# Optimization experiments

Hardware: AMD Instinct MI355X
Metric: run time of the kernel (lower is better)

The kernel has to match this reference:

```python
import jax, jax.numpy as jnp
import numpy as np

PROPOSAL_COUNT = 100
IOU_THRESHOLD = 0.5
SCORE_THRESHOLD = 0.05
IGNORE_LABEL = 0
PERFORMANCE_COUNT = 4096

B, N, C = 4, 100000, 80


def setup_inputs() -> dict:
    key = jax.random.key(0)
    k1, k2, k3, k4 = jax.random.split(key, 4)
    logits = jax.random.uniform(k1, (B, N, C), dtype=jnp.float32)
    regress = jax.random.uniform(k2, (B, N, 4), dtype=jnp.float32)
    points = jax.random.uniform(k3, (N, 2), dtype=jnp.float32)
    centerness = jax.random.uniform(k4, (B, N, 1), dtype=jnp.float32)
    return {"logits": logits, "regress": regress, "points": points, "centerness": centerness}


def offset2bbox(points, regress):
    return jnp.concatenate([points - regress[..., :2], points + regress[..., 2:]], axis=-1)


def pairwise_iou(boxes):
    # boxes: [K, 4] -> iou [K, K]
    area = (boxes[:, 2] - boxes[:, 0]) * (boxes[:, 3] - boxes[:, 1])
    lt = jnp.maximum(boxes[:, None, :2], boxes[None, :, :2])
    rb = jnp.minimum(boxes[:, None, 2:], boxes[None, :, 2:])
    wh = jnp.clip(rb - lt, 0.0)
    inter = wh[..., 0] * wh[..., 1]
    union = area[:, None] + area[None, :] - inter
    return inter / jnp.maximum(union, 1e-9)


def nms_image(logit, box):
    # logit: [N, C] (centerness-fused scores), box: [N, 4] decoded+clipped boxes
    n, c = logit.shape
    score = logit.at[:, IGNORE_LABEL].set(0.0)            # drop background class
    score = jnp.where(score > SCORE_THRESHOLD, score, 0.0)
    top_s, top_i = jax.lax.top_k(score.reshape(-1), PERFORMANCE_COUNT)  # over N*C pairs
    anchor = top_i // c
    cls = top_i % c
    cboxes = box[anchor]                                   # [K, 4]
    iou = pairwise_iou(cboxes)                             # [K, K]
    suppress = (iou > IOU_THRESHOLD) & (cls[:, None] == cls[None, :])

    def body(i, state):
        valid, sel = state
        s = jnp.where(valid, top_s, -1.0)
        j = jnp.argmax(s)
        ok = s[j] > 0.0
        sel = sel.at[i].set(jnp.where(ok, j.astype(jnp.int32), -1))
        valid = valid & ~suppress[j]
        valid = valid.at[j].set(False)
        return valid, sel

    valid0 = top_s > 0.0
    sel0 = jnp.full((PROPOSAL_COUNT,), -1, jnp.int32)
    _, sel = jax.lax.fori_loop(0, PROPOSAL_COUNT, body, (valid0, sel0))
    ok = sel >= 0
    selc = jnp.maximum(sel, 0)
    out_logit = jnp.where(ok[:, None], logit[anchor[selc]], 0.0)  # [P, C]
    out_box = jnp.where(ok[:, None], cboxes[selc], 0.0)           # [P, 4]
    return out_logit, out_box


def reference(logits, regress, points, centerness):
    fused = jnp.sqrt(logits * centerness)                        # centerness fusion
    boxes = jnp.clip(offset2bbox(points[None, :, :], regress), 0.0, 1.0)
    out_logit, out_box = jax.vmap(nms_image)(fused, boxes)
    return out_logit, out_box
```

## Files before the change

### kernel.cpp

```cpp
#include <hip/hip_runtime.h>
#include <cstdint>
#include <cstddef>

#define BB 4
#define NN 100000
#define CC 80
#define NC (NN * CC)
#define KTOP 4096
#define PROP 100
#define HBINS 10248
#define BUCKET_BASE 0x3D000u
#define CAPB 16384
#define SPILLCAP 131072
#define T0BK 0x3F733u
#define SPILL_LO (T0BK - BUCKET_BASE)
#define SPILL_BINS (HBINS - SPILL_LO)
#define P1CAP 1024
#define NSEL 512

#define HIST_BYTES (BB * HBINS * 4)
#define CTRL_OFF   HIST_BYTES
#define ZERO_BYTES (HIST_BYTES + 128)
#define CANDA_OFF  (HIST_BYTES + 128)
#define CANDB_OFF  (CANDA_OFF + BB * KTOP * 8)
#define SPILL_OFF  (CANDB_OFF + BB * CAPB * 8)
#define WS_NEEDED  ((size_t)SPILL_OFF + (size_t)BB * SPILLCAP * 8)

__device__ __forceinline__ void agg_push(bool pred, unsigned long long pk,
                                         unsigned* counter, unsigned long long* buf,
                                         unsigned cap, int lane) {
    unsigned long long m = __ballot(pred);
    if (m) {
        int leader = __ffsll(m) - 1;
        unsigned base = 0;
        if (lane == leader) base = atomicAdd(counter, (unsigned)__popcll(m));
        base = (unsigned)__shfl((int)base, leader);
        if (pred) {
            unsigned pos = base + (unsigned)__popcll(m & ((1ull << lane) - 1ull));
            if (pos < cap) buf[pos] = pk;
        }
    }
}

__global__ void k_pass1(const float* __restrict__ logits, const float* __restrict__ cent,
                        unsigned* __restrict__ ctrl, unsigned long long* __restrict__ spill) {
    int b = blockIdx.y;
    __shared__ unsigned long long lbuf[P1CAP];
    __shared__ unsigned lcnt, gbase, lflush;
    if (threadIdx.x == 0) lcnt = 0;
    __syncthreads();
    const float4* lg = (const float4*)(logits + (size_t)b * NC);
    const float* cb = cent + (size_t)b * NN;
    const int T4 = NC / 4;
    for (int i = blockIdx.x * blockDim.x + threadIdx.x; i < T4; i += gridDim.x * blockDim.x) {
        float4 v = lg[i];
        int n = i / 20;
        int c4 = (i - n * 20) * 4;
        float ce = cb[n];
        unsigned k0 = __float_as_uint(sqrtf(v.x * ce));
        unsigned k1 = __float_as_uint(sqrtf(v.y * ce));
        unsigned k2 = __float_as_uint(sqrtf(v.z * ce));
        unsigned k3 = __float_as_uint(sqrtf(v.w * ce));
        bool p0 = (c4 != 0) && ((k0 >> 12) >= T0BK);
        bool p1 = (k1 >> 12) >= T0BK;
        bool p2 = (k2 >> 12) >= T0BK;
        bool p3 = (k3 >> 12) >= T0BK;
        unsigned cnt = (unsigned)p0 + (unsigned)p1 + (unsigned)p2 + (unsigned)p3;
        if (cnt) {
            unsigned q = atomicAdd(&lcnt, cnt);
            unsigned f = (unsigned)i * 4u;
            if (p0) { if (q < P1CAP) lbuf[q] = ((unsigned long long)k0 << 32) | (unsigned)(~(f + 0)); q++; }
            if (p1) { if (q < P1CAP) lbuf[q] = ((unsigned long long)k1 << 32) | (unsigned)(~(f + 1)); q++; }
            if (p2) { if (q < P1CAP) lbuf[q] = ((unsigned long long)k2 << 32) | (unsigned)(~(f + 2)); q++; }
            if (p3) { if (q < P1CAP) lbuf[q] = ((unsigned long long)k3 << 32) | (unsigned)(~(f + 3)); }
        }
    }
    __syncthreads();
    if (threadIdx.x == 0) {
        unsigned n = lcnt;
        if (n > P1CAP) { atomicOr(&ctrl[6], 1u); n = P1CAP; }
        lflush = n;
        gbase = n ? atomicAdd(&ctrl[b * 8 + 4], n) : 0u;
    }
    __syncthreads();
    unsigned long long* sp = spill + (size_t)b * SPILLCAP;
    unsigned n = lflush, g0 = gbase;
    for (unsigned i = threadIdx.x; i < n; i += blockDim.x) {
        unsigned pos = g0 + i;
        if (pos < SPILLCAP) sp[pos] = lbuf[i];
    }
}

__global__ void k_slowflag(unsigned* __restrict__ ctrl) {
    if (threadIdx.x == 0 && blockIdx.x == 0) {
        unsigned f = ctrl[6] ? 1u : 0u;
        for (int b = 0; b < BB; b++) {
            unsigned ns = ctrl[b * 8 + 4];
            if (ns < KTOP || ns > SPILLCAP) f = 1;
        }
        ctrl[7] = f;
    }
}

__global__ void k_hist_spill(const unsigned* __restrict__ ctrl,
                             const unsigned long long* __restrict__ spill,
                             unsigned* __restrict__ hist) {
    if (ctrl[7]) return;
    int b = blockIdx.y;
    __shared__ unsigned lh[SPILL_BINS];
    for (int i = threadIdx.x; i < SPILL_BINS; i += blockDim.x) lh[i] = 0;
    __syncthreads();
    unsigned ns = ctrl[b * 8 + 4];
    if (ns > SPILLCAP) ns = SPILLCAP;
    const unsigned long long* sp = spill + (size_t)b * SPILLCAP;
    for (unsigned i = blockIdx.x * blockDim.x + threadIdx.x; i < ns; i += gridDim.x * blockDim.x) {
        unsigned bits = (unsigned)(sp[i] >> 32);
        atomicAdd(&lh[(bits >> 12) - T0BK], 1u);
    }
    __syncthreads();
    unsigned* gh = hist + (size_t)b * HBINS + SPILL_LO;
    for (int i = threadIdx.x; i < SPILL_BINS; i += blockDim.x) {
        unsigned c = lh[i];
        if (c) atomicAdd(&gh[i], c);
    }
}

__global__ void k_hist(const float* __restrict__ logits, const float* __restrict__ cent,
                       unsigned* __restrict__ hist, const unsigned* __restrict__ ctrl) {
    if (ctrl[7] == 0) return;
    int b = blockIdx.y;
    __shared__ unsigned lh[HBINS];
    for (int i = threadIdx.x; i < HBINS; i += blockDim.x) lh[i] = 0;
    __syncthreads();
    const float4* lg = (const float4*)(logits + (size_t)b * NC);
    const float* cb = cent + (size_t)b * NN;
    const int T4 = NC / 4;
    for (int i = blockIdx.x * blockDim.x + threadIdx.x; i < T4; i += gridDim.x * blockDim.x) {
        float4 v = lg[i];
        int n = i / 20;
        int c4 = (i - n * 20) * 4;
        float ce = cb[n];
        float s;
        s = sqrtf(v.x * ce);
        if (c4 != 0 && s > 0.05f) atomicAdd(&lh[(__float_as_uint(s) >> 12) - BUCKET_BASE], 1u);
        s = sqrtf(v.y * ce);
        if (s > 0.05f) atomicAdd(&lh[(__float_as_uint(s) >> 12) - BUCKET_BASE], 1u);
        s = sqrtf(v.z * ce);
        if (s > 0.05f) atomicAdd(&lh[(__float_as_uint(s) >> 12) - BUCKET_BASE], 1u);
        s = sqrtf(v.w * ce);
        if (s > 0.05f) atomicAdd(&lh[(__float_as_uint(s) >> 12) - BUCKET_BASE], 1u);
    }
    __syncthreads();
    unsigned* gh = hist + (size_t)b * HBINS;
    for (int i = threadIdx.x; i < HBINS; i += blockDim.x) {
        unsigned c = lh[i];
        if (c) atomicAdd(&gh[i], c);
    }
}

__global__ void k_select(const unsigned* __restrict__ hist, unsigned* __restrict__ ctrl) {
    int b = blockIdx.x;
    int t = threadIdx.x;
    const unsigned* h = hist + (size_t)b * HBINS;
    __shared__ unsigned ssum[256];
    const int CH = (HBINS + 255) / 256;
    unsigned acc0 = 0;
    for (int i = 0; i < CH; i++) {
        int idx = t * CH + i;
        if (idx < HBINS) acc0 += h[idx];
    }
    ssum[t] = acc0;
    __syncthreads();
    for (int off = 1; off < 256; off <<= 1) {
        unsigned v = (t + off < 256) ? ssum[t + off] : 0u;
        __syncthreads();
        ssum[t] += v;
        __syncthreads();
    }
    unsigned acc = (t < 255) ? ssum[t + 1] : 0u;
    for (int i = CH - 1; i >= 0; i--) {
        int idx = t * CH + i;
        if (idx >= HBINS) continue;
        unsigned cnt = h[idx];
        unsigned na = acc + cnt;
        if (na >= KTOP && acc < KTOP) {
            ctrl[b * 8 + 0] = (unsigned)idx;
            ctrl[b * 8 + 1] = acc;
        }
        acc = na;
    }
}

__global__ void k_compact_fast(unsigned* __restrict__ ctrl,
                               const unsigned long long* __restrict__ spill,
                               unsigned long long* __restrict__ candA,
                               unsigned long long* __restrict__ candB) {
    if (ctrl[7]) return;
    int b = blockIdx.y;
    unsigned B1 = ctrl[b * 8 + 0];
    unsigned ns = ctrl[b * 8 + 4];
    if (ns > SPILLCAP) ns = SPILLCAP;
    const unsigned long long* sp = spill + (size_t)b * SPILLCAP;
    unsigned long long* gA = candA + (size_t)b * KTOP;
    unsigned long long* gB = candB + (size_t)b * CAPB;
    int lane = threadIdx.x & 63;
    unsigned TT = gridDim.x * blockDim.x;
    unsigned iters = (ns + TT - 1) / TT;
    for (unsigned k2 = 0; k2 < iters; k2++) {
        unsigned i = k2 * TT + blockIdx.x * blockDim.x + threadIdx.x;
        bool active = (i < ns);
        unsigned long long pk = active ? sp[i] : 0ull;
        unsigned bk = active ? (((unsigned)(pk >> 32)) >> 12) - BUCKET_BASE : 0u;
        bool pA = active && (bk > B1);
        bool pB = active && (bk == B1);
        agg_push(pA, pk, &ctrl[b * 8 + 2], gA, KTOP, lane);
        agg_push(pB, pk, &ctrl[b * 8 + 3], gB, CAPB, lane);
    }
}

__global__ void k_compact(const float* __restrict__ logits, const float* __restrict__ cent,
                          unsigned* __restrict__ ctrl,
                          unsigned long long* __restrict__ candA,
                          unsigned long long* __restrict__ candB) {
    if (ctrl[7] == 0) return;
    int b = blockIdx.y;
    unsigned B1 = ctrl[b * 8 + 0];
    const float4* lg = (const float4*)(logits + (size_t)b * NC);
    const float* cb = cent + (size_t)b * NN;
    const int T4 = NC / 4;
    unsigned long long* gA = candA + (size_t)b * KTOP;
    unsigned long long* gB = candB + (size_t)b * CAPB;
    for (int i = blockIdx.x * blockDim.x + threadIdx.x; i < T4; i += gridDim.x * blockDim.x) {
        float4 v = lg[i];
        int n = i / 20;
        int c4 = (i - n * 20) * 4;
        float ce = cb[n];
        float sv[4] = {v.x, v.y, v.z, v.w};
#pragma unroll
        for (int k = 0; k < 4; k++) {
            float s = sqrtf(sv[k] * ce);
            int c = c4 + k;
            if (c != 0 && s > 0.05f) {
                unsigned key = __float_as_uint(s);
                unsigned bk = (key >> 12) - BUCKET_BASE;
                if (bk >= B1) {
                    unsigned flat = (unsigned)(i * 4 + k);
                    unsigned long long pk = ((unsigned long long)key << 32) | (unsigned)(~flat);
                    if (bk > B1) {
                        unsigned p = atomicAdd(&ctrl[b * 8 + 2], 1u);
                        if (p < KTOP) gA[p] = pk;
                    } else {
                        unsigned p = atomicAdd(&ctrl[b * 8 + 3], 1u);
                        if (p < CAPB) gB[p] = pk;
                    }
                }
            }
        }
    }
}

__global__ void k_boundary(unsigned* __restrict__ ctrl,
                           unsigned long long* __restrict__ candA,
                           const unsigned long long* __restrict__ candB) {
    int b = blockIdx.x;
    int t = threadIdx.x;
    unsigned nA = ctrl[b * 8 + 2];
    if (nA > KTOP) nA = KTOP;
    unsigned nB = ctrl[b * 8 + 3];
    if (nB > CAPB) nB = CAPB;
    int m = (int)KTOP - (int)nA;
    if (m < 0) m = 0;
    __shared__ unsigned long long sB[8192];
    const unsigned long long* gB = candB + (size_t)b * CAPB;
    unsigned long long* gA = candA + (size_t)b * KTOP;
    unsigned nBr = (nB + 255u) & ~255u;
    for (unsigned ii = 0; ii < nBr; ii += 256) {
        unsigned i = ii + (unsigned)t;
        bool act = (i < nB);
        unsigned long long ki = act ? gB[i] : 0ull;
        unsigned rank = 0;
        for (unsigned cb0 = 0; cb0 < nB; cb0 += 8192) {
            unsigned chunk = nB - cb0;
            if (chunk > 8192) chunk = 8192;
            __syncthreads();
            for (unsigned j = (unsigned)t; j < chunk; j += 256) sB[j] = gB[cb0 + j];
            __syncthreads();
            if (act) {
                for (unsigned j = 0; j < chunk; j++) rank += (sB[j] > ki) ? 1u : 0u;
            }
        }
        if (act && rank < (unsigned)m) gA[nA + rank] = ki;
    }
    unsigned take = ((unsigned)m < nB) ? (unsigned)m : nB;
    unsigned filled = nA + take;
    for (unsigned i = filled + (unsigned)t; i < KTOP; i += 256) gA[i] = 0ull;
}

__global__ void __launch_bounds__(256, 1) k_nms(const float* __restrict__ logits,
                                                const float* __restrict__ regress,
                                                const float* __restrict__ points,
                                                const float* __restrict__ cent,
                                                const unsigned long long* __restrict__ candA,
                                                float* __restrict__ out) {
    int b = blockIdx.x;
    int t = threadIdx.x;
    const unsigned long long* gA = candA + (size_t)b * KTOP;

    __shared__ unsigned long long sk[KTOP];
    __shared__ unsigned long long sel[KTOP];
    __shared__ float4 sbox[KTOP];
    __shared__ unsigned hist2[SPILL_BINS];
    __shared__ unsigned sc[8];
    __shared__ float4 kbox[PROP];
    __shared__ unsigned selAnc[PROP];

    for (int i = t; i < SPILL_BINS; i += 256) hist2[i] = 0;
    if (t < 8) sc[t] = 0;
    __syncthreads();
    for (int i = t; i < KTOP; i += 256) {
        unsigned long long kk = gA[i];
        sk[i] = kk;
        if (kk) {
            int bkt = (int)((unsigned)(kk >> 32) >> 12) - (int)T0BK;
            bkt = bkt < 0 ? 0 : bkt;
            atomicAdd(&hist2[bkt], 1u);
            atomicAdd(&sc[0], 1u);
        }
    }
    __syncthreads();

    for (int round = 0; round < 2; round++) {
        unsigned target = round == 0 ? NSEL : KTOP;
        if (t == 0) {
            unsigned total = sc[0];
            unsigned tgt = target < total ? target : total;
            int bq = SPILL_BINS;
            if (tgt > 0) {
                unsigned acc = 0;
                for (int i = SPILL_BINS - 1; i >= 0; i--) {
                    acc += hist2[i];
                    if (acc >= tgt) { bq = i; break; }
                }
            }
            sc[2] = (unsigned)bq;
            sc[1] = 0;
            sc[3] = 0;
            sc[4] = 0;
        }
        __syncthreads();
        int bq = (int)sc[2];
        for (int i = t; i < KTOP; i += 256) {
            unsigned long long kk = sk[i];
            if (kk) {
                int bkt = (int)((unsigned)(kk >> 32) >> 12) - (int)T0BK;
                bkt = bkt < 0 ? 0 : bkt;
                if (bkt >= bq) {
                    unsigned p = atomicAdd(&sc[1], 1u);
                    sel[p] = kk;
                }
            }
        }
        __syncthreads();
        unsigned S = sc[1];
        unsigned P2 = 2;
        while (P2 < S) P2 <<= 1;
        for (unsigned i = S + t; i < P2; i += 256) sel[i] = 0ull;
        __syncthreads();
        for (unsigned k = 2; k <= P2; k <<= 1) {
            for (unsigned j = k >> 1; j > 0; j >>= 1) {
                for (unsigned t2 = t; t2 < P2 / 2; t2 += 256) {
                    unsigned i = ((t2 & ~(j - 1)) << 1) | (t2 & (j - 1));
                    unsigned p2i = i + j;
                    bool dir = ((i & k) == 0);
                    unsigned long long a = sel[i], c = sel[p2i];
                    if ((a < c) == dir) { sel[i] = c; sel[p2i] = a; }
                }
                __syncthreads();
            }
        }
        for (unsigned i = t; i < S; i += 256) {
            unsigned long long kk = sel[i];
            float4 bx = {0.f, 0.f, 0.f, 0.f};
            if (kk) {
                unsigned flat = ~(unsigned)kk;
                unsigned a = flat / CC;
                float px = points[a * 2 + 0], py = points[a * 2 + 1];
                const float* rg = regress + ((size_t)b * NN + a) * 4;
                bx.x = fminf(fmaxf(px - rg[0], 0.f), 1.f);
                bx.y = fminf(fmaxf(py - rg[1], 0.f), 1.f);
                bx.z = fminf(fmaxf(px + rg[2], 0.f), 1.f);
                bx.w = fminf(fmaxf(py + rg[3], 0.f), 1.f);
            }
            sbox[i] = bx;
        }
        __syncthreads();
        if (t < 64) {
            int lane = t;
            float4 kb0 = {0, 0, 0, 0}, kb1 = {0, 0, 0, 0};
            unsigned kc0 = 0xFFFFFFFFu, kc1 = 0xFFFFFFFFu;
            int cnt = 0;
            for (unsigned i = 0; i < S && cnt < PROP; i++) {
                unsigned long long kk = sel[i];
                if (!kk) break;
                unsigned flat = ~(unsigned)kk;
                unsigned a = flat / CC;
                unsigned ccls = flat - a * CC;
                float4 c4 = sbox[i];
                float ca = (c4.z - c4.x) * (c4.w - c4.y);
                bool sup = false;
                if (lane < cnt && kc0 == ccls) {
                    float w = fmaxf(fminf(c4.z, kb0.z) - fmaxf(c4.x, kb0.x), 0.f);
                    float h = fmaxf(fminf(c4.w, kb0.w) - fmaxf(c4.y, kb0.y), 0.f);
                    float inter = w * h;
                    float ka = (kb0.z - kb0.x) * (kb0.w - kb0.y);
                    sup = inter / fmaxf(ca + ka - inter, 1e-9f) > 0.5f;
                }
                if (lane + 64 < cnt && kc1 == ccls) {
                    float w = fmaxf(fminf(c4.z, kb1.z) - fmaxf(c4.x, kb1.x), 0.f);
                    float h = fmaxf(fminf(c4.w, kb1.w) - fmaxf(c4.y, kb1.y), 0.f);
                    float inter = w * h;
                    float ka = (kb1.z - kb1.x) * (kb1.w - kb1.y);
                    sup = sup || (inter / fmaxf(ca + ka - inter, 1e-9f) > 0.5f);
                }
                if (!__any(sup)) {
                    if (lane == cnt) { kb0 = c4; kc0 = ccls; }
                    if (lane == cnt - 64) { kb1 = c4; kc1 = ccls; }
                    if (lane == 0) { kbox[cnt] = c4; selAnc[cnt] = a; }
                    cnt++;
                }
            }
            if (lane == 0) sc[3] = (unsigned)cnt;
        }
        __syncthreads();
        if (t == 0) sc[4] = (sc[3] < PROP && sc[1] < sc[0]) ? 1u : 0u;
        __syncthreads();
        if (!sc[4]) break;
    }

    unsigned nk = sc[3];
    float* outL = out + (size_t)b * PROP * CC;
    const float* lgb = logits + (size_t)b * NC;
    const float* cb = cent + (size_t)b * NN;
    for (int s = t; s < PROP * CC; s += 256) {
        int p = s / CC;
        int c = s - p * CC;
        float v = 0.f;
        if ((unsigned)p < nk) {
            unsigned a = selAnc[p];
            v = sqrtf(lgb[(size_t)a * CC + c] * cb[a]);
        }
        outL[s] = v;
    }
    float* outB = out + (size_t)BB * PROP * CC + (size_t)b * PROP * 4;
    for (int s = t; s < PROP * 4; s += 256) {
        int p = s >> 2;
        float v = 0.f;
        if ((unsigned)p < nk) v = ((const float*)&kbox[p])[s & 3];
        outB[s] = v;
    }
}

extern "C" void kernel_launch(void* const* d_in, const int* in_sizes, int n_in,
                              void* d_out, int out_size, void* d_ws, size_t ws_size,
                              hipStream_t stream) {
    const float* logits  = (const float*)d_in[0];
    const float* regress = (const float*)d_in[1];
    const float* points  = (const float*)d_in[2];
    const float* cent    = (const float*)d_in[3];
    float* out = (float*)d_out;

    char* ws = (char*)d_ws;
    unsigned* hist = (unsigned*)ws;
    unsigned* ctrl = (unsigned*)(ws + CTRL_OFF);
    unsigned long long* candA = (unsigned long long*)(ws + CANDA_OFF);
    unsigned long long* candB = (unsigned long long*)(ws + CANDB_OFF);
    unsigned long long* spill = (unsigned long long*)(ws + SPILL_OFF);

    hipMemsetAsync(d_ws, 0, ZERO_BYTES, stream);
    if (ws_size >= WS_NEEDED) {
        k_pass1<<<dim3(512, BB), 256, 0, stream>>>(logits, cent, ctrl, spill);
        k_slowflag<<<1, 64, 0, stream>>>(ctrl);
        k_hist_spill<<<dim3(32, BB), 256, 0, stream>>>(ctrl, spill, hist);
        k_hist<<<dim3(256, BB), 256, 0, stream>>>(logits, cent, hist, ctrl);
        k_select<<<BB, 256, 0, stream>>>(hist, ctrl);
        k_compact_fast<<<dim3(32, BB), 256, 0, stream>>>(ctrl, spill, candA, candB);
        k_compact<<<dim3(256, BB), 256, 0, stream>>>(logits, cent, ctrl, candA, candB);
    } else {
        hipMemsetAsync(ws + CTRL_OFF + 28, 1, 1, stream);
        k_hist<<<dim3(256, BB), 256, 0, stream>>>(logits, cent, hist, ctrl);
        k_select<<<BB, 256, 0, stream>>>(hist, ctrl);
        k_compact<<<dim3(256, BB), 256, 0, stream>>>(logits, cent, ctrl, candA, candB);
    }
    k_boundary<<<BB, 256, 0, stream>>>(ctrl, candA, candB);
    k_nms<<<BB, 256, 0, stream>>>(logits, regress, points, cent, candA, out);
}
```

Baseline: 329.0 us.

## Fuse select, compact, boundary and NMS into one per-image mega kernel

In the fast path, the top-K bucket selection, spill compaction, boundary ranking and NMS are merged into a single kernel with one block per image, so the separate k_compact_fast, k_boundary and k_nms launches go away. The first NMS round gathers only candidates at or above the NSEL quantile bucket straight from the spill buffer, deferring the full top-K and rank-append until a second round is needed. This cuts launch overhead and global round-trips. The cost is that work which previously ran across 32x4 blocks now runs in only 4 blocks, and there is a second scan of the spill.

```diff
diff --git a/kernel.cpp b/kernel.cpp
--- a/kernel.cpp
+++ b/kernel.cpp
@@ -25,22 +25,6 @@
 #define CANDB_OFF  (CANDA_OFF + BB * KTOP * 8)
 #define SPILL_OFF  (CANDB_OFF + BB * CAPB * 8)
 #define WS_NEEDED  ((size_t)SPILL_OFF + (size_t)BB * SPILLCAP * 8)
-
-__device__ __forceinline__ void agg_push(bool pred, unsigned long long pk,
-                                         unsigned* counter, unsigned long long* buf,
-                                         unsigned cap, int lane) {
-    unsigned long long m = __ballot(pred);
-    if (m) {
-        int leader = __ffsll(m) - 1;
-        unsigned base = 0;
-        if (lane == leader) base = atomicAdd(counter, (unsigned)__popcll(m));
-        base = (unsigned)__shfl((int)base, leader);
-        if (pred) {
-            unsigned pos = base + (unsigned)__popcll(m & ((1ull << lane) - 1ull));
-            if (pos < cap) buf[pos] = pk;
-        }
-    }
-}
 
 __global__ void k_pass1(const float* __restrict__ logits, const float* __restrict__ cent,
                         unsigned* __restrict__ ctrl, unsigned long long* __restrict__ spill) {
@@ -159,6 +143,7 @@
 }
 
 __global__ void k_select(const unsigned* __restrict__ hist, unsigned* __restrict__ ctrl) {
+    if (ctrl[7] == 0) return;
     int b = blockIdx.x;
     int t = threadIdx.x;
     const unsigned* h = hist + (size_t)b * HBINS;
@@ -188,33 +173,6 @@
             ctrl[b * 8 + 1] = acc;
         }
         acc = na;
-    }
-}
-
-__global__ void k_compact_fast(unsigned* __restrict__ ctrl,
-                               const unsigned long long* __restrict__ spill,
-                               unsigned long long* __restrict__ candA,
-                               unsigned long long* __restrict__ candB) {
-    if (ctrl[7]) return;
-    int b = blockIdx.y;
-    unsigned B1 = ctrl[b * 8 + 0];
-    unsigned ns = ctrl[b * 8 + 4];
-    if (ns > SPILLCAP) ns = SPILLCAP;
-    const unsigned long long* sp = spill + (size_t)b * SPILLCAP;
-    unsigned long long* gA = candA + (size_t)b * KTOP;
-    unsigned long long* gB = candB + (size_t)b * CAPB;
-    int lane = threadIdx.x & 63;
-    unsigned TT = gridDim.x * blockDim.x;
-    unsigned iters = (ns + TT - 1) / TT;
-    for (unsigned k2 = 0; k2 < iters; k2++) {
-        unsigned i = k2 * TT + blockIdx.x * blockDim.x + threadIdx.x;
-        bool active = (i < ns);
-        unsigned long long pk = active ? sp[i] : 0ull;
-        unsigned bk = active ? (((unsigned)(pk >> 32)) >> 12) - BUCKET_BASE : 0u;
-        bool pA = active && (bk > B1);
-        bool pB = active && (bk == B1);
-        agg_push(pA, pk, &ctrl[b * 8 + 2], gA, KTOP, lane);
-        agg_push(pB, pk, &ctrl[b * 8 + 3], gB, CAPB, lane);
     }
 }
 
@@ -259,125 +217,176 @@
     }
 }
 
-__global__ void k_boundary(unsigned* __restrict__ ctrl,
-                           unsigned long long* __restrict__ candA,
-                           const unsigned long long* __restrict__ candB) {
-    int b = blockIdx.x;
-    int t = threadIdx.x;
-    unsigned nA = ctrl[b * 8 + 2];
-    if (nA > KTOP) nA = KTOP;
-    unsigned nB = ctrl[b * 8 + 3];
-    if (nB > CAPB) nB = CAPB;
-    int m = (int)KTOP - (int)nA;
-    if (m < 0) m = 0;
-    __shared__ unsigned long long sB[8192];
-    const unsigned long long* gB = candB + (size_t)b * CAPB;
-    unsigned long long* gA = candA + (size_t)b * KTOP;
-    unsigned nBr = (nB + 255u) & ~255u;
-    for (unsigned ii = 0; ii < nBr; ii += 256) {
+__device__ void rank_append(const unsigned long long* gB, unsigned nb, unsigned m,
+                            unsigned long long* sel, unsigned Sbase,
+                            unsigned long long* scratch, int t) {
+    unsigned nbr = (nb + 255u) & ~255u;
+    for (unsigned ii = 0; ii < nbr; ii += 256) {
         unsigned i = ii + (unsigned)t;
-        bool act = (i < nB);
+        bool act = (i < nb);
         unsigned long long ki = act ? gB[i] : 0ull;
         unsigned rank = 0;
-        for (unsigned cb0 = 0; cb0 < nB; cb0 += 8192) {
-            unsigned chunk = nB - cb0;
+        for (unsigned c0 = 0; c0 < nb; c0 += 8192) {
+            unsigned chunk = nb - c0;
             if (chunk > 8192) chunk = 8192;
             __syncthreads();
-            for (unsigned j = (unsigned)t; j < chunk; j += 256) sB[j] = gB[cb0 + j];
+            for (unsigned j = (unsigned)t; j < chunk; j += 256) scratch[j] = gB[c0 + j];
             __syncthreads();
-            if (act) {
-                for (unsigned j = 0; j < chunk; j++) rank += (sB[j] > ki) ? 1u : 0u;
-            }
-        }
-        if (act && rank < (unsigned)m) gA[nA + rank] = ki;
-    }
-    unsigned take = ((unsigned)m < nB) ? (unsigned)m : nB;
-    unsigned filled = nA + take;
-    for (unsigned i = filled + (unsigned)t; i < KTOP; i += 256) gA[i] = 0ull;
-}
-
-__global__ void __launch_bounds__(256, 1) k_nms(const float* __restrict__ logits,
-                                                const float* __restrict__ regress,
-                                                const float* __restrict__ points,
-                                                const float* __restrict__ cent,
-                                                const unsigned long long* __restrict__ candA,
-                                                float* __restrict__ out) {
-    int b = blockIdx.x;
-    int t = threadIdx.x;
-    const unsigned long long* gA = candA + (size_t)b * KTOP;
-
-    __shared__ unsigned long long sk[KTOP];
+            if (act) for (unsigned j = 0; j < chunk; j++) rank += (scratch[j] > ki) ? 1u : 0u;
+        }
+        if (act && rank < m) sel[Sbase + rank] = ki;
+    }
+    __syncthreads();
+}
+
+__global__ void __launch_bounds__(256, 1) k_mega(
+    const float* __restrict__ logits, const float* __restrict__ regress,
+    const float* __restrict__ points, const float* __restrict__ cent,
+    const unsigned* __restrict__ hist, const unsigned* __restrict__ ctrl,
+    const unsigned long long* __restrict__ spill,
+    const unsigned long long* __restrict__ candA, unsigned long long* __restrict__ candB,
+    float* __restrict__ out) {
+    int b = blockIdx.x, t = threadIdx.x, lane = t & 63;
+    bool slow = ctrl[7] != 0;
     __shared__ unsigned long long sel[KTOP];
     __shared__ float4 sbox[KTOP];
-    __shared__ unsigned hist2[SPILL_BINS];
-    __shared__ unsigned sc[8];
+    __shared__ unsigned ssum[256];
     __shared__ float4 kbox[PROP];
     __shared__ unsigned selAnc[PROP];
-
-    for (int i = t; i < SPILL_BINS; i += 256) hist2[i] = 0;
-    if (t < 8) sc[t] = 0;
-    __syncthreads();
-    for (int i = t; i < KTOP; i += 256) {
-        unsigned long long kk = gA[i];
-        sk[i] = kk;
-        if (kk) {
-            int bkt = (int)((unsigned)(kk >> 32) >> 12) - (int)T0BK;
-            bkt = bkt < 0 ? 0 : bkt;
-            atomicAdd(&hist2[bkt], 1u);
-            atomicAdd(&sc[0], 1u);
-        }
-    }
-    __syncthreads();
+    __shared__ unsigned sv[8];
+    unsigned long long* scratch = (unsigned long long*)sbox;
+
+    const unsigned* h = hist + (size_t)b * HBINS;
+    const int CH = (HBINS + 255) / 256;
+    unsigned a0 = 0;
+    for (int i = 0; i < CH; i++) { int idx = t * CH + i; if (idx < HBINS) a0 += h[idx]; }
+    ssum[t] = a0;
+    __syncthreads();
+    for (int off = 1; off < 256; off <<= 1) {
+        unsigned v = (t + off < 256) ? ssum[t + off] : 0u;
+        __syncthreads(); ssum[t] += v; __syncthreads();
+    }
+    if (t == 0) { sv[0] = 0; sv[1] = 0; sv[2] = 0; }
+    __syncthreads();
+    unsigned acc = (t < 255) ? ssum[t + 1] : 0u;
+    for (int i = CH - 1; i >= 0; i--) {
+        int idx = t * CH + i;
+        if (idx >= HBINS) continue;
+        unsigned cnt = h[idx];
+        unsigned na = acc + cnt;
+        if (na >= KTOP && acc < KTOP) { sv[0] = (unsigned)idx; sv[1] = acc; }
+        if (na >= NSEL && acc < NSEL) { sv[2] = (unsigned)idx; }
+        acc = na;
+    }
+    __syncthreads();
+    unsigned B1 = slow ? ctrl[b * 8 + 0] : sv[0];
+    unsigned cntAbove = slow ? ctrl[b * 8 + 1] : sv[1];
+    unsigned Bq = sv[2];
+
+    const unsigned long long* sp = spill + (size_t)b * SPILLCAP;
+    const unsigned long long* gA = candA + (size_t)b * KTOP;
+    unsigned long long* gB = candB + (size_t)b * CAPB;
+    unsigned ns = 0, nA = 0;
+    if (!slow) { ns = ctrl[b * 8 + 4]; if (ns > SPILLCAP) ns = SPILLCAP; }
+    else       { nA = ctrl[b * 8 + 2]; if (nA > KTOP) nA = KTOP; }
+
+    unsigned S = 0, totalCand = 0, m = 0, nb = 0;
 
     for (int round = 0; round < 2; round++) {
-        unsigned target = round == 0 ? NSEL : KTOP;
-        if (t == 0) {
-            unsigned total = sc[0];
-            unsigned tgt = target < total ? target : total;
-            int bq = SPILL_BINS;
-            if (tgt > 0) {
-                unsigned acc = 0;
-                for (int i = SPILL_BINS - 1; i >= 0; i--) {
-                    acc += hist2[i];
-                    if (acc >= tgt) { bq = i; break; }
-                }
-            }
-            sc[2] = (unsigned)bq;
-            sc[1] = 0;
-            sc[3] = 0;
-            sc[4] = 0;
-        }
-        __syncthreads();
-        int bq = (int)sc[2];
-        for (int i = t; i < KTOP; i += 256) {
-            unsigned long long kk = sk[i];
-            if (kk) {
-                int bkt = (int)((unsigned)(kk >> 32) >> 12) - (int)T0BK;
-                bkt = bkt < 0 ? 0 : bkt;
-                if (bkt >= bq) {
-                    unsigned p = atomicAdd(&sc[1], 1u);
-                    sel[p] = kk;
-                }
-            }
-        }
-        __syncthreads();
-        unsigned S = sc[1];
+        if (t == 0) { sv[4] = 0; sv[5] = 0; sv[6] = 0; if (round == 0) sv[7] = 0; }
+        __syncthreads();
+        bool full = (round == 1) || (Bq <= B1);
+
+        if (!slow) {
+            for (unsigned i = t; i < ns; i += 256) {
+                unsigned long long k = sp[i];
+                unsigned bkt = ((unsigned)(k >> 32) >> 12) - BUCKET_BASE;
+                bool psel = full ? (bkt > B1) : (bkt >= Bq);
+                unsigned long long mm = __ballot(psel);
+                if (mm) {
+                    int ld = __ffsll(mm) - 1;
+                    unsigned base = 0;
+                    if (lane == ld) base = atomicAdd(&sv[4], (unsigned)__popcll(mm));
+                    base = (unsigned)__shfl((int)base, ld);
+                    if (psel) {
+                        unsigned pos = base + (unsigned)__popcll(mm & ((1ull << lane) - 1ull));
+                        if (pos < KTOP) sel[pos] = k;
+                    }
+                }
+                if (round == 0) {
+                    bool pb = (bkt == B1);
+                    unsigned long long mb = __ballot(pb);
+                    if (mb) {
+                        int ld = __ffsll(mb) - 1;
+                        unsigned base = 0;
+                        if (lane == ld) base = atomicAdd(&sv[7], (unsigned)__popcll(mb));
+                        base = (unsigned)__shfl((int)base, ld);
+                        if (pb) {
+                            unsigned pos = base + (unsigned)__popcll(mb & ((1ull << lane) - 1ull));
+                            if (pos < CAPB) gB[pos] = k;
+                        }
+                    }
+                }
+            }
+            __syncthreads();
+            if (round == 0) {
+                nb = sv[7]; if (nb > CAPB) nb = CAPB;
+                unsigned cA = (Bq <= B1) ? sv[4] : cntAbove;
+                if (cA > KTOP) cA = KTOP;
+                m = (cA < KTOP) ? (KTOP - cA) : 0;
+                if (m > nb) m = nb;
+                totalCand = cA + m;
+                if (totalCand > KTOP) totalCand = KTOP;
+            }
+        } else {
+            for (unsigned i = t; i < nA; i += 256) {
+                unsigned long long k = gA[i];
+                unsigned bkt = ((unsigned)(k >> 32) >> 12) - BUCKET_BASE;
+                bool psel = full || (bkt >= Bq);
+                unsigned long long mm = __ballot(psel);
+                if (mm) {
+                    int ld = __ffsll(mm) - 1;
+                    unsigned base = 0;
+                    if (lane == ld) base = atomicAdd(&sv[4], (unsigned)__popcll(mm));
+                    base = (unsigned)__shfl((int)base, ld);
+                    if (psel) {
+                        unsigned pos = base + (unsigned)__popcll(mm & ((1ull << lane) - 1ull));
+                        if (pos < KTOP) sel[pos] = k;
+                    }
+                }
+            }
+            __syncthreads();
+            if (round == 0) {
+                nb = ctrl[b * 8 + 3]; if (nb > CAPB) nb = CAPB;
+                m = (nA < KTOP) ? (KTOP - nA) : 0;
+                if (m > nb) m = nb;
+                totalCand = nA + m;
+            }
+        }
+        S = sv[4]; if (S > KTOP) S = KTOP;
+        if (full && m > 0 && S + m <= KTOP) {
+            rank_append(gB, nb, m, sel, S, scratch, t);
+            S += m;
+        }
+        __syncthreads();
+
         unsigned P2 = 2;
         while (P2 < S) P2 <<= 1;
         for (unsigned i = S + t; i < P2; i += 256) sel[i] = 0ull;
         __syncthreads();
-        for (unsigned k = 2; k <= P2; k <<= 1) {
-            for (unsigned j = k >> 1; j > 0; j >>= 1) {
+        for (unsigned k2 = 2; k2 <= P2; k2 <<= 1) {
+            for (unsigned j = k2 >> 1; j > 0; j >>= 1) {
                 for (unsigned t2 = t; t2 < P2 / 2; t2 += 256) {
                     unsigned i = ((t2 & ~(j - 1)) << 1) | (t2 & (j - 1));
                     unsigned p2i = i + j;
-                    bool dir = ((i & k) == 0);
+                    bool dir = ((i & k2) == 0);
                     unsigned long long a = sel[i], c = sel[p2i];
                     if ((a < c) == dir) { sel[i] = c; sel[p2i] = a; }
                 }
                 __syncthreads();
             }
         }
+
         for (unsigned i = t; i < S; i += 256) {
             unsigned long long kk = sel[i];
             float4 bx = {0.f, 0.f, 0.f, 0.f};
@@ -394,8 +403,8 @@
             sbox[i] = bx;
         }
         __syncthreads();
+
         if (t < 64) {
-            int lane = t;
             float4 kb0 = {0, 0, 0, 0}, kb1 = {0, 0, 0, 0};
             unsigned kc0 = 0xFFFFFFFFu, kc1 = 0xFFFFFFFFu;
             int cnt = 0;
@@ -410,15 +419,15 @@
                 bool sup = false;
                 if (lane < cnt && kc0 == ccls) {
                     float w = fmaxf(fminf(c4.z, kb0.z) - fmaxf(c4.x, kb0.x), 0.f);
-                    float h = fmaxf(fminf(c4.w, kb0.w) - fmaxf(c4.y, kb0.y), 0.f);
-                    float inter = w * h;
+                    float hh = fmaxf(fminf(c4.w, kb0.w) - fmaxf(c4.y, kb0.y), 0.f);
+                    float inter = w * hh;
                     float ka = (kb0.z - kb0.x) * (kb0.w - kb0.y);
                     sup = inter / fmaxf(ca + ka - inter, 1e-9f) > 0.5f;
                 }
                 if (lane + 64 < cnt && kc1 == ccls) {
                     float w = fmaxf(fminf(c4.z, kb1.z) - fmaxf(c4.x, kb1.x), 0.f);
-                    float h = fmaxf(fminf(c4.w, kb1.w) - fmaxf(c4.y, kb1.y), 0.f);
-                    float inter = w * h;
+                    float hh = fmaxf(fminf(c4.w, kb1.w) - fmaxf(c4.y, kb1.y), 0.f);
+                    float inter = w * hh;
                     float ka = (kb1.z - kb1.x) * (kb1.w - kb1.y);
                     sup = sup || (inter / fmaxf(ca + ka - inter, 1e-9f) > 0.5f);
                 }
@@ -429,15 +438,15 @@
                     cnt++;
                 }
             }
-            if (lane == 0) sc[3] = (unsigned)cnt;
-        }
-        __syncthreads();
-        if (t == 0) sc[4] = (sc[3] < PROP && sc[1] < sc[0]) ? 1u : 0u;
-        __syncthreads();
-        if (!sc[4]) break;
-    }
-
-    unsigned nk = sc[3];
+            if (lane == 0) sv[5] = (unsigned)cnt;
+        }
+        __syncthreads();
+        if (t == 0) sv[6] = (sv[5] < PROP && S < totalCand) ? 1u : 0u;
+        __syncthreads();
+        if (!sv[6]) break;
+    }
+
+    unsigned nk = sv[5];
     float* outL = out + (size_t)b * PROP * CC;
     const float* lgb = logits + (size_t)b * NC;
     const float* cb = cent + (size_t)b * NN;
@@ -483,7 +492,6 @@
         k_hist_spill<<<dim3(32, BB), 256, 0, stream>>>(ctrl, spill, hist);
         k_hist<<<dim3(256, BB), 256, 0, stream>>>(logits, cent, hist, ctrl);
         k_select<<<BB, 256, 0, stream>>>(hist, ctrl);
-        k_compact_fast<<<dim3(32, BB), 256, 0, stream>>>(ctrl, spill, candA, candB);
         k_compact<<<dim3(256, BB), 256, 0, stream>>>(logits, cent, ctrl, candA, candB);
     } else {
         hipMemsetAsync(ws + CTRL_OFF + 28, 1, 1, stream);
@@ -491,6 +499,5 @@
         k_select<<<BB, 256, 0, stream>>>(hist, ctrl);
         k_compact<<<dim3(256, BB), 256, 0, stream>>>(logits, cent, ctrl, candA, candB);
     }
-    k_boundary<<<BB, 256, 0, stream>>>(ctrl, candA, candB);
-    k_nms<<<BB, 256, 0, stream>>>(logits, regress, points, cent, candA, out);
-}
+    k_mega<<<BB, 256, 0, stream>>>(logits, regress, points, cent, hist, ctrl, spill, candA, candB, out);
+}
```

Result: slower. 355.7 us (+8.1%).
